# Optimization experiments

Measured on AMD Instinct MI355X. Metric: run time of the kernel, lower is better.

The kernel has to match this reference:

```python
import jax, jax.numpy as jnp
import numpy as np

EMA_OLD = 0.01  # original: m[z] = m[z]*0.01 + y*0.99
EMA_NEW = 0.99

def setup_inputs() -> dict:
    key = jax.random.key(0)
    k1, k2, k3, k4 = jax.random.split(key, 4)
    B, n, C, L = 4096, 1024, 64, 64
    y = jax.random.normal(k1, (B, C, L), dtype=jnp.float32)   # encoder latents
    m = jax.random.normal(k2, (n, C, L), dtype=jnp.float32)   # codebook means
    sd = jax.random.uniform(k3, (n, C, L), dtype=jnp.float32) # codebook variances (init ones in orig)
    p = jax.random.uniform(k4, (n,), dtype=jnp.float32)       # cluster counts
    return {"y": y, "m": m, "sd": sd, "p": p}

def reference(y, m, sd, p):
    B, C, L = y.shape
    n = m.shape[0]
    # pairwise squared distances via ||y||^2 - 2 y.m + ||m||^2 (GEMM form)
    yf = y.reshape(B, C * L)
    mf = m.reshape(n, C * L)
    d2 = ((yf * yf).sum(-1, keepdims=True)
          - 2.0 * (yf @ mf.T)
          + (mf * mf).sum(-1)[None, :])            # [B, n]
    z = jnp.argmin(d2, axis=1)                      # [B] assignments
    new_m = m.at[z].set(m[z] * EMA_OLD + y * EMA_NEW)
    # original updates sd using the ALREADY-updated m gathered at z
    mg = new_m[z]
    new_sd = sd.at[z].set((mg - y) ** 2 * EMA_OLD + sd[z] * EMA_NEW)
    return jnp.concatenate([new_m, new_sd], axis=0)  # [2n, C, L]
```

## Files before the change

kernel.cpp:

```cpp
#include <hip/hip_runtime.h>

#define B_ROWS 4096
#define N_CLUST 1024
#define KDIM 4096
#define NKT 32
#define NSTEP 16

#define EMA_OLD 0.01f
#define EMA_NEW 0.99f
#define MARGIN 2.0f
#define PSCALE 16.0f
#define PLANE ((size_t)B_ROWS * N_CLUST)

typedef unsigned short ushortT;
typedef _Float16 half8 __attribute__((ext_vector_type(8)));
typedef short short8v __attribute__((ext_vector_type(8)));
typedef float f32x16 __attribute__((ext_vector_type(16)));

#define WS_WINNER_OFF 0
#define WS_YY_OFF     20480
#define WS_MM_OFF     36864
#define WS_P_OFF      65536
#define WS_YHI_OFF    (WS_P_OFF + 33554432)
#define WS_MHI_OFF    (WS_YHI_OFF + 33554432)
#define WS_END        (WS_MHI_OFF + 8388608)

__global__ __launch_bounds__(256) void convert_sumsq(
    const float* __restrict__ ysrc, const float* __restrict__ msrc,
    ushortT* __restrict__ yhi, ushortT* __restrict__ mhi,
    float* __restrict__ yy, float* __restrict__ mm,
    int* __restrict__ winner) {
    const int blk = blockIdx.x;
    const float* src;
    ushortT* hi;
    float* out;
    int row;
    if (blk < B_ROWS) {
        src = ysrc; hi = yhi; out = yy + blk; row = blk;
    } else {
        row = blk - B_ROWS;
        src = msrc; hi = mhi; out = mm + row;
        if (threadIdx.x == 0) winner[row] = -1;
    }
    const int r = row & 63, rb = row >> 6;
    const int t = threadIdx.x;
    float s = 0.f;
#pragma unroll
    for (int h = 0; h < 2; ++h) {
        int ci = h * 256 + t;
        int kt = ci >> 4, p = ci & 15;
        int c = p ^ (r & 15);
        const float* sp = src + ((size_t)row << 12) + kt * 128 + c * 8;
        float4 v0 = *(const float4*)sp;
        float4 v1 = *(const float4*)(sp + 4);
        float vv[8] = {v0.x, v0.y, v0.z, v0.w, v1.x, v1.y, v1.z, v1.w};
        half8 hv;
#pragma unroll
        for (int i = 0; i < 8; ++i) {
            hv[i] = (_Float16)vv[i];
            s += vv[i] * vv[i];
        }
        size_t off = (((size_t)rb * NKT + kt) * 64 + r) * 128 + p * 8;
        *(half8*)(hi + off) = hv;
    }
    for (int off = 32; off > 0; off >>= 1) s += __shfl_down(s, off, 64);
    __shared__ float red[4];
    if ((t & 63) == 0) red[t >> 6] = s;
    __syncthreads();
    if (t == 0) out[0] = red[0] + red[1] + red[2] + red[3];
}

__device__ __forceinline__ void gload_lds16(const void* g, void* l) {
    __builtin_amdgcn_global_load_lds(
        (const __attribute__((address_space(1))) unsigned int*)g,
        (__attribute__((address_space(3))) unsigned int*)l, 16, 0, 0);
}

__device__ __forceinline__ half8 ldfrag_pair(const ushortT* s, int r, int c) {
    int q = r >> 1;
    int sl = ((((r & 1) << 3) | c) ^ (q & 15));
    return *(const half8*)(s + q * 128 + sl * 8);
}

__global__ __launch_bounds__(256, 4) void screen_gemm(
    const ushortT* __restrict__ Ah, const ushortT* __restrict__ Bh,
    short* __restrict__ pws) {
    __shared__ __align__(16) ushortT sA[128 * 64];
    __shared__ __align__(16) ushortT sB[128 * 64];

    const int t = threadIdx.x, w = t >> 6, l = t & 63;
    const int by = blockIdx.x & 7;
    const int kh = (blockIdx.x >> 3) & 3;
    const int bx = blockIdx.x >> 5;
    const int row0 = bx * 128, col0 = by * 128;
    const int wr = (w >> 1) * 64, wc = (w & 1) * 64;
    const int m0 = l & 31, hsel = l >> 5;

    int laneoff[4];
#pragma unroll
    for (int j = 0; j < 4; ++j) {
        int g = w * 4 + j;
        int q = g * 4 + (l >> 4);
        int u = (l & 15) ^ (q & 15);
        int rr = 2 * q + (u >> 3);
        int R = rr & 63;
        int hi3 = (R >> 3) & 1;
        laneoff[j] = R * 256 + ((((hi3 << 3) | ((u & 7) ^ (R & 7)))) << 4);
    }

    f32x16 acc[2][2];
#pragma unroll
    for (int i = 0; i < 2; ++i)
#pragma unroll
        for (int j = 0; j < 2; ++j)
#pragma unroll
            for (int r = 0; r < 16; ++r) acc[i][j][r] = 0.f;

    const int ra0 = wr + m0, ra1 = wr + 32 + m0;
    const int rb0 = wc + m0, rb1 = wc + 32 + m0;

#pragma unroll 2
    for (int i = 0; i < NSTEP; ++i) {
        const int kt_ = kh * (NKT / 4) + (i >> 1);
        const int ks_ = i & 1;
        __syncthreads();
#pragma unroll
        for (int j = 0; j < 4; ++j) {
            const int g = w * 4 + j;
            const int lo = laneoff[j] ^ (ks_ << 7);
            const size_t tbA = ((size_t)((2 * bx + (g >> 3)) * NKT + kt_) << 14);
            const size_t tbB = ((size_t)((2 * by + (g >> 3)) * NKT + kt_) << 14);
            gload_lds16((const char*)Ah + tbA + lo, (char*)sA + g * 1024);
            gload_lds16((const char*)Bh + tbB + lo, (char*)sB + g * 1024);
        }
        __syncthreads();

#pragma unroll
        for (int kk = 0; kk < 4; ++kk) {
            int c = kk * 2 + hsel;
            half8 a0 = ldfrag_pair(sA, ra0, c);
            half8 a1 = ldfrag_pair(sA, ra1, c);
            half8 b0 = ldfrag_pair(sB, rb0, c);
            half8 b1 = ldfrag_pair(sB, rb1, c);
            acc[0][0] = __builtin_amdgcn_mfma_f32_32x32x16_f16(a0, b0, acc[0][0], 0, 0, 0);
            acc[0][1] = __builtin_amdgcn_mfma_f32_32x32x16_f16(a0, b1, acc[0][1], 0, 0, 0);
            acc[1][0] = __builtin_amdgcn_mfma_f32_32x32x16_f16(a1, b0, acc[1][0], 0, 0, 0);
            acc[1][1] = __builtin_amdgcn_mfma_f32_32x32x16_f16(a1, b1, acc[1][1], 0, 0, 0);
        }
    }

    short* pk = pws + (size_t)kh * PLANE;
#pragma unroll
    for (int i = 0; i < 2; ++i)
#pragma unroll
        for (int j = 0; j < 2; ++j) {
            const int gcol = col0 + wc + j * 32 + m0;
#pragma unroll
            for (int r = 0; r < 16; ++r) {
                int ri = (r & 3) + 8 * (r >> 2) + 4 * hsel;
                int grow = row0 + wr + i * 32 + ri;
                float q = fmaxf(fminf(acc[i][j][r] * (-2.0f * PSCALE),
                                      32767.f), -32767.f);
                pk[(size_t)grow * N_CLUST + gcol] = (short)__float2int_rn(q);
            }
        }
}

__global__ __launch_bounds__(256) void rescreen(
    const short* __restrict__ pws, const float* __restrict__ ysrc,
    const float* __restrict__ msrc, const float* __restrict__ yy,
    const float* __restrict__ mm, int* __restrict__ winner) {
    const int row = blockIdx.x * 4 + (threadIdx.x >> 6);
    const int l = threadIdx.x & 63;
    const size_t rb = (size_t)row * N_CLUST;

    int sacc[16];
#pragma unroll
    for (int q = 0; q < 16; ++q) sacc[q] = 0;
    const short* base = pws + rb + l * 16;
#pragma unroll
    for (int pl = 0; pl < 4; ++pl) {
        const short8v* sp = (const short8v*)(base + pl * PLANE);
        short8v x0 = sp[0], x1 = sp[1];
#pragma unroll
        for (int e = 0; e < 8; ++e) {
            sacc[e] += (int)x0[e];
            sacc[8 + e] += (int)x1[e];
        }
    }
    float v[16];
    const float4* mmv = (const float4*)(mm + l * 16);
#pragma unroll
    for (int h = 0; h < 4; ++h) {
        float4 mv = mmv[h];
        v[h * 4 + 0] = mv.x + (float)sacc[h * 4 + 0] * (1.0f / PSCALE);
        v[h * 4 + 1] = mv.y + (float)sacc[h * 4 + 1] * (1.0f / PSCALE);
        v[h * 4 + 2] = mv.z + (float)sacc[h * 4 + 2] * (1.0f / PSCALE);
        v[h * 4 + 3] = mv.w + (float)sacc[h * 4 + 3] * (1.0f / PSCALE);
    }

    float m1 = v[0], m2 = 3.0e38f;
    int a1 = l * 16;
#pragma unroll
    for (int q = 1; q < 16; ++q) {
        float x = v[q];
        if (x < m1) { m2 = m1; m1 = x; a1 = l * 16 + q; }
        else m2 = fminf(m2, x);
    }
#pragma unroll
    for (int s = 1; s <= 32; s <<= 1) {
        float o1 = __shfl_xor(m1, s, 64);
        int ob = __shfl_xor(a1, s, 64);
        float o2 = __shfl_xor(m2, s, 64);
        if (o1 < m1 || (o1 == m1 && ob < a1)) {
            m2 = fminf(o2, m1); m1 = o1; a1 = ob;
        } else {
            m2 = fminf(m2, o1);
        }
    }

    int zj;
    if (m2 - m1 > MARGIN) {
        zj = a1;
    } else {
        const float thr = m1 + MARGIN;
        double bestd = 1e300;
        int bestj = 0x7FFFFFFF;
        const float yyr = yy[row];
        const float4* yp = (const float4*)(ysrc + (size_t)row * KDIM);
        for (int q = 0; q < 16; ++q) {
            unsigned long long mask = __ballot(v[q] <= thr);
            while (mask) {
                int lb = __ffsll((unsigned long long)mask) - 1;
                mask &= mask - 1;
                int j = lb * 16 + q;
                const float4* mp = (const float4*)(msrc + (size_t)j * KDIM);
                double acc = 0.0;
#pragma unroll
                for (int tt = 0; tt < 16; ++tt) {
                    float4 a = yp[l + 64 * tt];
                    float4 b = mp[l + 64 * tt];
                    acc += (double)a.x * b.x + (double)a.y * b.y +
                           (double)a.z * b.z + (double)a.w * b.w;
                }
#pragma unroll
                for (int s = 1; s <= 32; s <<= 1)
                    acc += __shfl_xor(acc, s, 64);
                double d2x = (double)yyr - 2.0 * acc + (double)mm[j];
                if (d2x < bestd || (d2x == bestd && j < bestj)) {
                    bestd = d2x; bestj = j;
                }
            }
        }
        zj = bestj;
    }
    if (l == 0) atomicMax(&winner[zj], row);
}

__global__ __launch_bounds__(256) void write_out(
    const float* __restrict__ y, const float* __restrict__ m,
    const float* __restrict__ sd, const int* __restrict__ winner,
    float* __restrict__ out) {
    const int idx = blockIdx.x;
    const int t = threadIdx.x;
    const int w = winner[idx];
    const float4* mp = (const float4*)(m + (size_t)idx * KDIM);
    const float4* sp = (const float4*)(sd + (size_t)idx * KDIM);
    float4* om = (float4*)(out + (size_t)idx * KDIM);
    float4* os = (float4*)(out + (size_t)(N_CLUST + idx) * KDIM);
    if (w >= 0) {
        const float4* yp = (const float4*)(y + (size_t)w * KDIM);
        for (int i = t; i < KDIM / 4; i += 256) {
            float4 mv = mp[i], yv = yp[i], sv = sp[i];
            float4 nm, ns;
            nm.x = mv.x * EMA_OLD + yv.x * EMA_NEW;
            nm.y = mv.y * EMA_OLD + yv.y * EMA_NEW;
            nm.z = mv.z * EMA_OLD + yv.z * EMA_NEW;
            nm.w = mv.w * EMA_OLD + yv.w * EMA_NEW;
            float dx = nm.x - yv.x, dy = nm.y - yv.y;
            float dz = nm.z - yv.z, dw = nm.w - yv.w;
            ns.x = dx * dx * EMA_OLD + sv.x * EMA_NEW;
            ns.y = dy * dy * EMA_OLD + sv.y * EMA_NEW;
            ns.z = dz * dz * EMA_OLD + sv.z * EMA_NEW;
            ns.w = dw * dw * EMA_OLD + sv.w * EMA_NEW;
            om[i] = nm;
            os[i] = ns;
        }
    } else {
        for (int i = t; i < KDIM / 4; i += 256) {
            om[i] = mp[i];
            os[i] = sp[i];
        }
    }
}

extern "C" void kernel_launch(void* const* d_in, const int* in_sizes, int n_in,
                              void* d_out, int out_size, void* d_ws,
                              size_t ws_size, hipStream_t stream) {
    const float* y  = (const float*)d_in[0];
    const float* m  = (const float*)d_in[1];
    const float* sd = (const float*)d_in[2];
    float* out = (float*)d_out;

    char* ws = (char*)d_ws;
    int* winner = (int*)(ws + WS_WINNER_OFF);
    float* yy   = (float*)(ws + WS_YY_OFF);
    float* mm   = (float*)(ws + WS_MM_OFF);
    short* pws  = (short*)(ws + WS_P_OFF);
    ushortT* yhi = (ushortT*)(ws + WS_YHI_OFF);
    ushortT* mhi = (ushortT*)(ws + WS_MHI_OFF);

    convert_sumsq<<<B_ROWS + N_CLUST, 256, 0, stream>>>(
        y, m, yhi, mhi, yy, mm, winner);

    screen_gemm<<<(B_ROWS / 128) * (N_CLUST / 128) * 4, 256, 0, stream>>>(
        yhi, mhi, pws);

    rescreen<<<B_ROWS / 4, 256, 0, stream>>>(pws, y, m, yy, mm, winner);

    write_out<<<N_CLUST, 256, 0, stream>>>(y, m, sd, winner, out);
}
```

Baseline: 215.4 us.

## Double-buffer screen GEMM LDS tiles and halve split-K partial planes

The screen GEMM now keeps two LDS buffers per operand and issues the global-to-LDS loads for the next K step before computing the current one. It waits with a partial vmcnt and raises wave priority around the MFMA block, so global loads overlap compute. Split-K drops from 4 to 2, which halves the partial-sum planes written and then re-read by rescreen. In exchange LDS use doubles, occupancy drops to 2 blocks per CU, and the grid shrinks to 512 blocks, which lowers parallelism.

```diff
diff --git a/kernel.cpp b/kernel.cpp
--- a/kernel.cpp
+++ b/kernel.cpp
@@ -4,7 +4,7 @@
 #define N_CLUST 1024
 #define KDIM 4096
 #define NKT 32
-#define NSTEP 16
+#define NSTEP 32
 
 #define EMA_OLD 0.01f
 #define EMA_NEW 0.99f
@@ -82,16 +82,16 @@
     return *(const half8*)(s + q * 128 + sl * 8);
 }
 
-__global__ __launch_bounds__(256, 4) void screen_gemm(
+__global__ __launch_bounds__(256, 2) void screen_gemm(
     const ushortT* __restrict__ Ah, const ushortT* __restrict__ Bh,
     short* __restrict__ pws) {
-    __shared__ __align__(16) ushortT sA[128 * 64];
-    __shared__ __align__(16) ushortT sB[128 * 64];
+    __shared__ __align__(16) ushortT sA[2][128 * 64];
+    __shared__ __align__(16) ushortT sB[2][128 * 64];
 
     const int t = threadIdx.x, w = t >> 6, l = t & 63;
     const int by = blockIdx.x & 7;
-    const int kh = (blockIdx.x >> 3) & 3;
-    const int bx = blockIdx.x >> 5;
+    const int kh = (blockIdx.x >> 3) & 1;
+    const int bx = blockIdx.x >> 4;
     const int row0 = bx * 128, col0 = by * 128;
     const int wr = (w >> 1) * 64, wc = (w & 1) * 64;
     const int m0 = l & 31, hsel = l >> 5;
@@ -119,35 +119,58 @@
     const int ra0 = wr + m0, ra1 = wr + 32 + m0;
     const int rb0 = wc + m0, rb1 = wc + 32 + m0;
 
+#define STAGE(buf, step)                                                      \
+    {                                                                         \
+        const int kt_ = kh * (NKT / 2) + ((step) >> 1);                       \
+        const int ks_ = (step) & 1;                                           \
+        _Pragma("unroll")                                                     \
+        for (int j = 0; j < 4; ++j) {                                         \
+            const int g = w * 4 + j;                                          \
+            const int lo = laneoff[j] ^ (ks_ << 7);                           \
+            const size_t tbA =                                                \
+                ((size_t)((2 * bx + (g >> 3)) * NKT + kt_) << 14);            \
+            const size_t tbB =                                                \
+                ((size_t)((2 * by + (g >> 3)) * NKT + kt_) << 14);            \
+            gload_lds16((const char*)Ah + tbA + lo,                           \
+                        (char*)&sA[buf][0] + g * 1024);                       \
+            gload_lds16((const char*)Bh + tbB + lo,                           \
+                        (char*)&sB[buf][0] + g * 1024);                       \
+        }                                                                     \
+    }
+
+    STAGE(0, 0);
+
 #pragma unroll 2
     for (int i = 0; i < NSTEP; ++i) {
-        const int kt_ = kh * (NKT / 4) + (i >> 1);
-        const int ks_ = i & 1;
-        __syncthreads();
-#pragma unroll
-        for (int j = 0; j < 4; ++j) {
-            const int g = w * 4 + j;
-            const int lo = laneoff[j] ^ (ks_ << 7);
-            const size_t tbA = ((size_t)((2 * bx + (g >> 3)) * NKT + kt_) << 14);
-            const size_t tbB = ((size_t)((2 * by + (g >> 3)) * NKT + kt_) << 14);
-            gload_lds16((const char*)Ah + tbA + lo, (char*)sA + g * 1024);
-            gload_lds16((const char*)Bh + tbB + lo, (char*)sB + g * 1024);
-        }
-        __syncthreads();
-
+        const int buf = i & 1;
+        if (i + 1 < NSTEP) {
+            STAGE(buf ^ 1, i + 1);
+            asm volatile("s_waitcnt vmcnt(8)" ::: "memory");
+        } else {
+            asm volatile("s_waitcnt vmcnt(0)" ::: "memory");
+        }
+        __builtin_amdgcn_s_barrier();
+
+        const ushortT* tA = &sA[buf][0];
+        const ushortT* tB = &sB[buf][0];
+        __builtin_amdgcn_s_setprio(1);
 #pragma unroll
         for (int kk = 0; kk < 4; ++kk) {
             int c = kk * 2 + hsel;
-            half8 a0 = ldfrag_pair(sA, ra0, c);
-            half8 a1 = ldfrag_pair(sA, ra1, c);
-            half8 b0 = ldfrag_pair(sB, rb0, c);
-            half8 b1 = ldfrag_pair(sB, rb1, c);
+            half8 a0 = ldfrag_pair(tA, ra0, c);
+            half8 a1 = ldfrag_pair(tA, ra1, c);
+            half8 b0 = ldfrag_pair(tB, rb0, c);
+            half8 b1 = ldfrag_pair(tB, rb1, c);
             acc[0][0] = __builtin_amdgcn_mfma_f32_32x32x16_f16(a0, b0, acc[0][0], 0, 0, 0);
             acc[0][1] = __builtin_amdgcn_mfma_f32_32x32x16_f16(a0, b1, acc[0][1], 0, 0, 0);
             acc[1][0] = __builtin_amdgcn_mfma_f32_32x32x16_f16(a1, b0, acc[1][0], 0, 0, 0);
             acc[1][1] = __builtin_amdgcn_mfma_f32_32x32x16_f16(a1, b1, acc[1][1], 0, 0, 0);
         }
-    }
+        __builtin_amdgcn_s_setprio(0);
+        asm volatile("" ::: "memory");
+        __builtin_amdgcn_s_barrier();
+    }
+#undef STAGE
 
     short* pk = pws + (size_t)kh * PLANE;
 #pragma unroll
@@ -179,7 +202,7 @@
     for (int q = 0; q < 16; ++q) sacc[q] = 0;
     const short* base = pws + rb + l * 16;
 #pragma unroll
-    for (int pl = 0; pl < 4; ++pl) {
+    for (int pl = 0; pl < 2; ++pl) {
         const short8v* sp = (const short8v*)(base + pl * PLANE);
         short8v x0 = sp[0], x1 = sp[1];
 #pragma unroll
@@ -313,7 +336,7 @@
     convert_sumsq<<<B_ROWS + N_CLUST, 256, 0, stream>>>(
         y, m, yhi, mhi, yy, mm, winner);
 
-    screen_gemm<<<(B_ROWS / 128) * (N_CLUST / 128) * 4, 256, 0, stream>>>(
+    screen_gemm<<<(B_ROWS / 128) * (N_CLUST / 128) * 2, 256, 0, stream>>>(
         yhi, mhi, pws);
 
     rescreen<<<B_ROWS / 4, 256, 0, stream>>>(pws, y, m, yy, mm, winner);
```

Result: no change. 214.1 us (-0.6%).
